# Kernel tuning notes

Hardware: AMD Instinct MI355X
Metric: run time of the kernel (lower is better)

The kernel has to match this reference:

```python
import jax, jax.numpy as jnp
import numpy as np
from jax import lax

KERNEL = 3
EPS = 0.01


def _box_sum(x, k):
    # sum over kxk window, stride 1, SAME-style explicit padding of k//2
    pad = k // 2
    return lax.reduce_window(
        x, 0.0, lax.add,
        window_dimensions=(1, 1, k, k),
        window_strides=(1, 1, 1, 1),
        padding=((0, 0), (0, 0), (pad, pad), (pad, pad)),
    )


def _box_counts(h, w, k, dtype):
    # number of valid (non-padded) elements in each window (count_include_pad=False)
    ones = jnp.ones((1, 1, h, w), dtype=dtype)
    return _box_sum(ones, k)


def _blur(x, counts, k):
    return _box_sum(x, k) / counts


def setup_inputs() -> dict:
    key = jax.random.key(0)
    k1, k2 = jax.random.split(key)
    shape = (8, 16, 512, 512)
    inp = jax.random.normal(k1, shape, dtype=jnp.float32)
    guide = jax.random.normal(k2, shape, dtype=jnp.float32)
    return {"input": inp, "guide": guide}


def reference(input, guide):
    I, p = input, guide
    B, C, H, W = I.shape
    counts = _box_counts(H, W, KERNEL, I.dtype)  # [1,1,H,W]

    mean_I = _blur(I, counts, KERNEL)
    mean_p = _blur(p, counts, KERNEL)
    mean_II = _blur(I * I, counts, KERNEL)
    mean_Ip = _blur(I * p, counts, KERNEL)

    var_I = mean_II - mean_I * mean_I
    cov_Ip = mean_Ip - mean_I * mean_p

    a = cov_Ip / (var_I + EPS)
    b = mean_p - a * mean_I

    mean_a = _blur(a, counts, KERNEL)
    mean_b = _blur(b, counts, KERNEL)

    return mean_a * I + mean_b
```

## Files before the change

### kernel.cpp

```cpp
#include <hip/hip_runtime.h>


constexpr int W  = 512;
constexpr int H  = 512;
constexpr int TW = 64;
constexpr int TH = 16;
constexpr int IPH = TH + 4;
constexpr int IPW = TW + 4;
constexpr int ABH = TH + 2;
constexpr int ABW = TW + 2;
constexpr float EPS  = 0.01f;
constexpr float INV9 = 1.0f / 9.0f;

template<bool INT>
__device__ __forceinline__ void run_tile(
    const float* __restrict__ Ibase, const float* __restrict__ Pbase,
    float* __restrict__ Obase, int x0, int y0, int tid,
    float2 (*sIP)[IPW], float2 (*sAB)[ABW])
{
    if (INT) {
        for (int t = tid; t < 34 * IPH; t += 256) {
            const int row = t / 34;
            const int pc  = t - row * 34;
            const int g   = (y0 - 2 + row) * W + (x0 - 2 + 2 * pc);
            const float2 vi = *(const float2*)(Ibase + g);
            const float2 vp = *(const float2*)(Pbase + g);
            *(float4*)&sIP[row][2 * pc] = make_float4(vi.x, vp.x, vi.y, vp.y);
        }
    } else {
        for (int t = tid; t < 34 * IPH; t += 256) {
            const int row = t / 34;
            const int pc  = t - row * 34;
            const int gy  = y0 - 2 + row;
            const int gx  = x0 - 2 + 2 * pc;
            float i0 = 0.f, i1 = 0.f, q0 = 0.f, q1 = 0.f;
            if (gy >= 0 && gy < H) {
                const int g = gy * W + gx;
                if (gx >= 0 && gx + 1 < W) {
                    const float2 vi = *(const float2*)(Ibase + g);
                    const float2 vp = *(const float2*)(Pbase + g);
                    i0 = vi.x; i1 = vi.y; q0 = vp.x; q1 = vp.y;
                } else {
                    if ((unsigned)gx < (unsigned)W)       { i0 = Ibase[g];     q0 = Pbase[g]; }
                    if ((unsigned)(gx + 1) < (unsigned)W) { i1 = Ibase[g + 1]; q1 = Pbase[g + 1]; }
                }
            }
            *(float4*)&sIP[row][2 * pc] = make_float4(i0, q0, i1, q1);
        }
    }
    __syncthreads();

    if (tid < 99) {
        const int p    = tid % 33;
        const int s    = tid / 33;
        const int row0 = 6 * s;

        float hI[2][3], hP[2][3], hII[2][3], hIP[2][3];
        #pragma unroll
        for (int j = 0; j < 8; ++j) {
            const int rr = row0 + j;
            const float4 c01 = *(const float4*)&sIP[rr][2 * p];
            const float4 c23 = *(const float4*)&sIP[rr][2 * p + 2];
            const float i0 = c01.x, q0 = c01.y, i1 = c01.z, q1 = c01.w;
            const float i2 = c23.x, q2 = c23.y, i3 = c23.z, q3 = c23.w;
            const int k = j % 3;
            const float tI  = i1 + i2, tP = q1 + q2;
            const float tII = fmaf(i1, i1, i2 * i2);
            const float tIP = fmaf(i1, q1, i2 * q2);
            hI[0][k]  = tI + i0;            hI[1][k]  = tI + i3;
            hP[0][k]  = tP + q0;            hP[1][k]  = tP + q3;
            hII[0][k] = fmaf(i0, i0, tII);  hII[1][k] = fmaf(i3, i3, tII);
            hIP[0][k] = fmaf(i0, q0, tIP);  hIP[1][k] = fmaf(i3, q3, tIP);
            if (j >= 2) {
                const int ay = row0 + j - 2;
                float ab[4];
                #pragma unroll
                for (int c = 0; c < 2; ++c) {
                    const float wI  = hI[c][0]  + hI[c][1]  + hI[c][2];
                    const float wP  = hP[c][0]  + hP[c][1]  + hP[c][2];
                    const float wII = hII[c][0] + hII[c][1] + hII[c][2];
                    const float wIP = hIP[c][0] + hIP[c][1] + hIP[c][2];
                    float a = 0.f, b = 0.f;
                    if (INT) {
                        const float mI   = wI * INV9, mP = wP * INV9;
                        const float varI = fmaf(-mI, mI, wII * INV9);
                        const float cov  = fmaf(-mI, mP, wIP * INV9);
                        a = cov * __builtin_amdgcn_rcpf(varI + EPS);
                        b = fmaf(-a, mI, mP);
                    } else {
                        const int gx = x0 - 1 + 2 * p + c;
                        const int gy = y0 - 1 + ay;
                        if ((unsigned)gx < (unsigned)W && (unsigned)gy < (unsigned)H) {
                            const float cx = 3.f - (float)(gx == 0) - (float)(gx == W - 1);
                            const float cy = 3.f - (float)(gy == 0) - (float)(gy == H - 1);
                            const float inv  = __builtin_amdgcn_rcpf(cx * cy);
                            const float mI   = wI * inv, mP = wP * inv;
                            const float varI = fmaf(-mI, mI, wII * inv);
                            const float cov  = fmaf(-mI, mP, wIP * inv);
                            a = cov * __builtin_amdgcn_rcpf(varI + EPS);
                            b = fmaf(-a, mI, mP);
                        }
                    }
                    ab[2 * c] = a; ab[2 * c + 1] = b;
                }
                *(float4*)&sAB[ay][2 * p] = make_float4(ab[0], ab[1], ab[2], ab[3]);
            }
        }
    }
    __syncthreads();

    if (tid < 128) {
        const int q   = tid & 31;
        const int r   = tid >> 5;
        const int ox0 = 2 * q;
        const int oy0 = 4 * r;
        float hA[2][3], hB[2][3];
        #pragma unroll
        for (int j = 0; j < 6; ++j) {
            const float4 c01 = *(const float4*)&sAB[oy0 + j][ox0];
            const float4 c23 = *(const float4*)&sAB[oy0 + j][ox0 + 2];
            const float a0 = c01.x, b0 = c01.y, a1 = c01.z, b1 = c01.w;
            const float a2 = c23.x, b2 = c23.y, a3 = c23.z, b3 = c23.w;
            const int k = j % 3;
            const float tA = a1 + a2, tB = b1 + b2;
            hA[0][k] = tA + a0; hA[1][k] = tA + a3;
            hB[0][k] = tB + b0; hB[1][k] = tB + b3;
            if (j >= 2) {
                const int oy = oy0 + j - 2;
                const int gy = y0 + oy;
                const int go = gy * W + x0 + ox0;
                const float2 iv = *(const float2*)(Ibase + go);
                float res[2];
                #pragma unroll
                for (int c = 0; c < 2; ++c) {
                    const float sa = hA[c][0] + hA[c][1] + hA[c][2];
                    const float sb = hB[c][0] + hB[c][1] + hB[c][2];
                    float inv;
                    if (INT) {
                        inv = INV9;
                    } else {
                        const int gx = x0 + ox0 + c;
                        const float cx = 3.f - (float)(gx == 0) - (float)(gx == W - 1);
                        const float cy = 3.f - (float)(gy == 0) - (float)(gy == H - 1);
                        inv = __builtin_amdgcn_rcpf(cx * cy);
                    }
                    const float Ic = (c == 0) ? iv.x : iv.y;
                    res[c] = fmaf(sa * inv, Ic, sb * inv);
                }
                *(float2*)(Obase + go) = make_float2(res[0], res[1]);
            }
        }
    }
}

__global__ __launch_bounds__(256, 7) void guide_filter_kernel(
    const float* __restrict__ I, const float* __restrict__ P,
    float* __restrict__ O)
{
    __shared__ __align__(16) float2 sIP[IPH][IPW];
    __shared__ __align__(16) float2 sAB[ABH][ABW];

    const int tid = threadIdx.x;
    const int x0  = blockIdx.x * TW;
    const int y0  = blockIdx.y * TH;
    const size_t img_off = (size_t)blockIdx.z * (size_t)(W * H);
    const bool interior = (blockIdx.x > 0) & (blockIdx.x < gridDim.x - 1) &
                          (blockIdx.y > 0) & (blockIdx.y < gridDim.y - 1);
    if (interior) {
        run_tile<true >(I + img_off, P + img_off, (float*)O + img_off, x0, y0, tid, sIP, sAB);
    } else {
        run_tile<false>(I + img_off, P + img_off, (float*)O + img_off, x0, y0, tid, sIP, sAB);
    }
}

extern "C" void kernel_launch(void* const* d_in, const int* in_sizes, int n_in,
                              void* d_out, int out_size, void* d_ws, size_t ws_size,
                              hipStream_t stream) {
    const float* I = (const float*)d_in[0];
    const float* P = (const float*)d_in[1];
    float*       O = (float*)d_out;
    const int images = in_sizes[0] / (W * H);
    dim3 grid(W / TW, H / TH, images);
    guide_filter_kernel<<<grid, dim3(256), 0, stream>>>(I, P, O);
}
```

Baseline: 319.7 us.

## Load input halo directly from global into registers, drop input shared tile

```diff
diff --git a/kernel.cpp b/kernel.cpp
--- a/kernel.cpp
+++ b/kernel.cpp
@@ -5,8 +5,6 @@
 constexpr int H  = 512;
 constexpr int TW = 64;
 constexpr int TH = 16;
-constexpr int IPH = TH + 4;
-constexpr int IPW = TW + 4;
 constexpr int ABH = TH + 2;
 constexpr int ABW = TW + 2;
 constexpr float EPS  = 0.01f;
@@ -16,53 +14,48 @@
 __device__ __forceinline__ void run_tile(
     const float* __restrict__ Ibase, const float* __restrict__ Pbase,
     float* __restrict__ Obase, int x0, int y0, int tid,
-    float2 (*sIP)[IPW], float2 (*sAB)[ABW])
+    float2 (*sAB)[ABW])
 {
-    if (INT) {
-        for (int t = tid; t < 34 * IPH; t += 256) {
-            const int row = t / 34;
-            const int pc  = t - row * 34;
-            const int g   = (y0 - 2 + row) * W + (x0 - 2 + 2 * pc);
-            const float2 vi = *(const float2*)(Ibase + g);
-            const float2 vp = *(const float2*)(Pbase + g);
-            *(float4*)&sIP[row][2 * pc] = make_float4(vi.x, vp.x, vi.y, vp.y);
-        }
-    } else {
-        for (int t = tid; t < 34 * IPH; t += 256) {
-            const int row = t / 34;
-            const int pc  = t - row * 34;
-            const int gy  = y0 - 2 + row;
-            const int gx  = x0 - 2 + 2 * pc;
-            float i0 = 0.f, i1 = 0.f, q0 = 0.f, q1 = 0.f;
-            if (gy >= 0 && gy < H) {
-                const int g = gy * W + gx;
-                if (gx >= 0 && gx + 1 < W) {
-                    const float2 vi = *(const float2*)(Ibase + g);
-                    const float2 vp = *(const float2*)(Pbase + g);
-                    i0 = vi.x; i1 = vi.y; q0 = vp.x; q1 = vp.y;
-                } else {
-                    if ((unsigned)gx < (unsigned)W)       { i0 = Ibase[g];     q0 = Pbase[g]; }
-                    if ((unsigned)(gx + 1) < (unsigned)W) { i1 = Ibase[g + 1]; q1 = Pbase[g + 1]; }
-                }
-            }
-            *(float4*)&sIP[row][2 * pc] = make_float4(i0, q0, i1, q1);
-        }
-    }
-    __syncthreads();
-
-    if (tid < 99) {
-        const int p    = tid % 33;
-        const int s    = tid / 33;
-        const int row0 = 6 * s;
+    if (tid < 198) {
+        const int s   = tid / 33;
+        const int p   = tid - 33 * s;
+        const int ay0 = 3 * s;
+        const int gx  = x0 - 2 + 2 * p;
+        const int gy0 = y0 - 2 + ay0;
 
         float hI[2][3], hP[2][3], hII[2][3], hIP[2][3];
         #pragma unroll
-        for (int j = 0; j < 8; ++j) {
-            const int rr = row0 + j;
-            const float4 c01 = *(const float4*)&sIP[rr][2 * p];
-            const float4 c23 = *(const float4*)&sIP[rr][2 * p + 2];
-            const float i0 = c01.x, q0 = c01.y, i1 = c01.z, q1 = c01.w;
-            const float i2 = c23.x, q2 = c23.y, i3 = c23.z, q3 = c23.w;
+        for (int j = 0; j < 5; ++j) {
+            const int gy = gy0 + j;
+            float i0, i1, i2, i3, q0, q1, q2, q3;
+            if (INT) {
+                const int g = gy * W + gx;
+                const float2 a01 = *(const float2*)(Ibase + g);
+                const float2 a23 = *(const float2*)(Ibase + g + 2);
+                const float2 b01 = *(const float2*)(Pbase + g);
+                const float2 b23 = *(const float2*)(Pbase + g + 2);
+                i0 = a01.x; i1 = a01.y; i2 = a23.x; i3 = a23.y;
+                q0 = b01.x; q1 = b01.y; q2 = b23.x; q3 = b23.y;
+            } else {
+                i0 = i1 = i2 = i3 = 0.f; q0 = q1 = q2 = q3 = 0.f;
+                if ((unsigned)gy < (unsigned)H) {
+                    const float* Ir = Ibase + gy * W;
+                    const float* Pr = Pbase + gy * W;
+                    if (gx >= 0 && gx + 3 < W) {
+                        const float2 a01 = *(const float2*)(Ir + gx);
+                        const float2 a23 = *(const float2*)(Ir + gx + 2);
+                        const float2 b01 = *(const float2*)(Pr + gx);
+                        const float2 b23 = *(const float2*)(Pr + gx + 2);
+                        i0 = a01.x; i1 = a01.y; i2 = a23.x; i3 = a23.y;
+                        q0 = b01.x; q1 = b01.y; q2 = b23.x; q3 = b23.y;
+                    } else {
+                        if ((unsigned)(gx + 0) < (unsigned)W) { i0 = Ir[gx + 0]; q0 = Pr[gx + 0]; }
+                        if ((unsigned)(gx + 1) < (unsigned)W) { i1 = Ir[gx + 1]; q1 = Pr[gx + 1]; }
+                        if ((unsigned)(gx + 2) < (unsigned)W) { i2 = Ir[gx + 2]; q2 = Pr[gx + 2]; }
+                        if ((unsigned)(gx + 3) < (unsigned)W) { i3 = Ir[gx + 3]; q3 = Pr[gx + 3]; }
+                    }
+                }
+            }
             const int k = j % 3;
             const float tI  = i1 + i2, tP = q1 + q2;
             const float tII = fmaf(i1, i1, i2 * i2);
@@ -72,7 +65,7 @@
             hII[0][k] = fmaf(i0, i0, tII);  hII[1][k] = fmaf(i3, i3, tII);
             hIP[0][k] = fmaf(i0, q0, tIP);  hIP[1][k] = fmaf(i3, q3, tIP);
             if (j >= 2) {
-                const int ay = row0 + j - 2;
+                const int ay = ay0 + j - 2;
                 float ab[4];
                 #pragma unroll
                 for (int c = 0; c < 2; ++c) {
@@ -88,11 +81,11 @@
                         a = cov * __builtin_amdgcn_rcpf(varI + EPS);
                         b = fmaf(-a, mI, mP);
                     } else {
-                        const int gx = x0 - 1 + 2 * p + c;
-                        const int gy = y0 - 1 + ay;
-                        if ((unsigned)gx < (unsigned)W && (unsigned)gy < (unsigned)H) {
-                            const float cx = 3.f - (float)(gx == 0) - (float)(gx == W - 1);
-                            const float cy = 3.f - (float)(gy == 0) - (float)(gy == H - 1);
+                        const int axg = x0 - 1 + 2 * p + c;
+                        const int ayg = y0 - 1 + ay;
+                        if ((unsigned)axg < (unsigned)W && (unsigned)ayg < (unsigned)H) {
+                            const float cx = 3.f - (float)(axg == 0) - (float)(axg == W - 1);
+                            const float cy = 3.f - (float)(ayg == 0) - (float)(ayg == H - 1);
                             const float inv  = __builtin_amdgcn_rcpf(cx * cy);
                             const float mI   = wI * inv, mP = wP * inv;
                             const float varI = fmaf(-mI, mI, wII * inv);
@@ -109,14 +102,14 @@
     }
     __syncthreads();
 
-    if (tid < 128) {
+    {
         const int q   = tid & 31;
         const int r   = tid >> 5;
         const int ox0 = 2 * q;
-        const int oy0 = 4 * r;
+        const int oy0 = 2 * r;
         float hA[2][3], hB[2][3];
         #pragma unroll
-        for (int j = 0; j < 6; ++j) {
+        for (int j = 0; j < 4; ++j) {
             const float4 c01 = *(const float4*)&sAB[oy0 + j][ox0];
             const float4 c23 = *(const float4*)&sAB[oy0 + j][ox0 + 2];
             const float a0 = c01.x, b0 = c01.y, a1 = c01.z, b1 = c01.w;
@@ -139,8 +132,8 @@
                     if (INT) {
                         inv = INV9;
                     } else {
-                        const int gx = x0 + ox0 + c;
-                        const float cx = 3.f - (float)(gx == 0) - (float)(gx == W - 1);
+                        const int gxo = x0 + ox0 + c;
+                        const float cx = 3.f - (float)(gxo == 0) - (float)(gxo == W - 1);
                         const float cy = 3.f - (float)(gy == 0) - (float)(gy == H - 1);
                         inv = __builtin_amdgcn_rcpf(cx * cy);
                     }
@@ -153,11 +146,10 @@
     }
 }
 
-__global__ __launch_bounds__(256, 7) void guide_filter_kernel(
+__global__ __launch_bounds__(256, 8) void guide_filter_kernel(
     const float* __restrict__ I, const float* __restrict__ P,
     float* __restrict__ O)
 {
-    __shared__ __align__(16) float2 sIP[IPH][IPW];
     __shared__ __align__(16) float2 sAB[ABH][ABW];
 
     const int tid = threadIdx.x;
@@ -167,9 +159,9 @@
     const bool interior = (blockIdx.x > 0) & (blockIdx.x < gridDim.x - 1) &
                           (blockIdx.y > 0) & (blockIdx.y < gridDim.y - 1);
     if (interior) {
-        run_tile<true >(I + img_off, P + img_off, (float*)O + img_off, x0, y0, tid, sIP, sAB);
+        run_tile<true >(I + img_off, P + img_off, (float*)O + img_off, x0, y0, tid, sAB);
     } else {
-        run_tile<false>(I + img_off, P + img_off, (float*)O + img_off, x0, y0, tid, sIP, sAB);
+        run_tile<false>(I + img_off, P + img_off, (float*)O + img_off, x0, y0, tid, sAB);
     }
 }
 
```

New measurement: 358.2 us. +12.1%, slower.
